# Performance work log

Measured on AMD Instinct MI355X. Metric: run time of the kernel, lower is better.

Reference implementation:

```python
import jax, jax.numpy as jnp
import numpy as np

NEG_SLOPE = 0.2  # PyG GATConv default negative_slope


def gat_conv(x, edge_index, W, att_src, att_dst, bias):
    """PyG-style GATConv (concat heads, add_self_loops=True, eval mode).
    x: [N, F_in], edge_index: [2, E] (row 0 = src j, row 1 = dst i).
    W: [F_in, H*C], att_src/att_dst: [H, C], bias: [H*C].
    """
    N = x.shape[0]
    H, C = att_src.shape
    loops = jnp.arange(N, dtype=edge_index.dtype)
    src = jnp.concatenate([edge_index[0], loops])  # [E+N]
    dst = jnp.concatenate([edge_index[1], loops])
    h = (x @ W).reshape(N, H, C)                              # [N,H,C]
    a_src = jnp.einsum('nhc,hc->nh', h, att_src)              # [N,H]
    a_dst = jnp.einsum('nhc,hc->nh', h, att_dst)
    alpha = jax.nn.leaky_relu(a_src[src] + a_dst[dst], NEG_SLOPE)  # [E+N,H]
    # segment softmax over edges sharing the same destination node
    m = jax.ops.segment_max(alpha, dst, num_segments=N)       # [N,H]
    e = jnp.exp(alpha - jax.lax.stop_gradient(m)[dst])
    denom = jax.ops.segment_sum(e, dst, num_segments=N)       # [N,H]
    a = e / (denom[dst] + 1e-16)                              # [E+N,H]
    msg = h[src] * a[:, :, None]                              # [E+N,H,C]
    out = jax.ops.segment_sum(msg, dst, num_segments=N)       # [N,H,C]
    return out.reshape(N, H * C) + bias


def setup_inputs() -> dict:
    key = jax.random.key(0)
    ks = jax.random.split(key, 10)
    N, F, NC, C1, H1 = 50000, 128, 40, 16, 8
    E = 800000
    x = jax.random.normal(ks[0], (N, F), dtype=jnp.float32)
    edge_index = jax.random.randint(ks[1], (2, E), 0, N, dtype=jnp.int64)
    s1 = 1.0 / np.sqrt(F)
    W1 = jax.random.uniform(ks[2], (F, H1 * C1), jnp.float32, -s1, s1)
    att_src1 = jax.random.uniform(ks[3], (H1, C1), jnp.float32, -1.0, 1.0) * s1
    att_dst1 = jax.random.uniform(ks[4], (H1, C1), jnp.float32, -1.0, 1.0) * s1
    bias1 = jnp.zeros((H1 * C1,), jnp.float32)
    s2 = 1.0 / np.sqrt(H1 * C1)
    W2 = jax.random.uniform(ks[5], (H1 * C1, NC), jnp.float32, -s2, s2)
    att_src2 = jax.random.uniform(ks[6], (1, NC), jnp.float32, -1.0, 1.0) * s2
    att_dst2 = jax.random.uniform(ks[7], (1, NC), jnp.float32, -1.0, 1.0) * s2
    bias2 = jnp.zeros((NC,), jnp.float32)
    return {"x": x, "edge_index": edge_index, "W1": W1, "att_src1": att_src1,
            "att_dst1": att_dst1, "bias1": bias1, "W2": W2, "att_src2": att_src2,
            "att_dst2": att_dst2, "bias2": bias2}


def reference(x, edge_index, W1, att_src1, att_dst1, bias1, W2, att_src2, att_dst2, bias2):
    h = gat_conv(x, edge_index, W1, att_src1, att_dst1, bias1)   # [N, 128]
    # dropout in eval mode = identity
    out = gat_conv(h, edge_index, W2, att_src2, att_dst2, bias2)  # [N, 40]
    return out
```

## Files before the change

### kernel.cpp

```cpp
#include <hip/hip_runtime.h>
#include <hip/hip_bf16.h>
#include <math.h>

#define NEG_SLOPE 0.2f
#define WSZ 384
#define GZ  32

typedef __bf16 bf16x8 __attribute__((ext_vector_type(8)));
typedef float f32x4 __attribute__((ext_vector_type(4)));

__device__ __forceinline__ float lrelu(float x) { return x > 0.f ? x : NEG_SLOPE * x; }

__device__ __forceinline__ unsigned short f2bfu(float f) {
    unsigned int ua = __float_as_uint(f);
    return (unsigned short)((ua + 0x7fffu + ((ua >> 16) & 1u)) >> 16);
}
__device__ __forceinline__ float bfu2f(unsigned short u) {
    return __uint_as_float(((unsigned int)u) << 16);
}
__device__ __forceinline__ float bf_lo(unsigned int u) { return __uint_as_float(u << 16); }
__device__ __forceinline__ float bf_hi(unsigned int u) { return __uint_as_float(u & 0xffff0000u); }

__global__ __launch_bounds__(256) void k_prep(const float* __restrict__ W1,
                                              bf16x8* __restrict__ Wp,
                                              const float* __restrict__ W2,
                                              bf16x8* __restrict__ W2p,
                                              const float* __restrict__ att_s1,
                                              const float* __restrict__ att_d1,
                                              const float* __restrict__ att_s2,
                                              const float* __restrict__ att_d2,
                                              int* __restrict__ cnt, int N) {
    int g = blockIdx.x * 256 + threadIdx.x;
    if (g < 2048) {
        int n = g & 15, quad = (g >> 4) & 3, c = (g >> 6) & 3, ct = g >> 8;
        bf16x8 v;
#pragma unroll
        for (int j = 0; j < 8; ++j)
            v[j] = (__bf16)W1[(c * 32 + quad * 8 + j) * 128 + ct * 16 + n];
        Wp[g] = v;
    } else if (g < 2560) {
        int idx = g - 2048;
        int n = idx & 15, quad = (idx >> 4) & 3, c = (idx >> 6) & 3, t8 = idx >> 8;
        int h = n & 7;
        const float* av = (n < 8) ? att_s1 : att_d1;
        bf16x8 vv;
#pragma unroll
        for (int j = 0; j < 8; ++j) {
            int f = c * 32 + quad * 8 + j;
            float full = 0.f;
            for (int cc = 0; cc < 16; ++cc)
                full += W1[f * 128 + h * 16 + cc] * av[h * 16 + cc];
            __bf16 hi = (__bf16)full;
            vv[j] = t8 ? (__bf16)(full - (float)hi) : hi;
        }
        Wp[g] = vv;
    } else if (g < 3328) {
        int idx = g - 2560;
        int n = idx & 15, quad = (idx >> 4) & 3, c = (idx >> 6) & 3, ct = idx >> 8;
        int colc = ct * 16 + n;
        bf16x8 v;
        if (colc < 40) {
#pragma unroll
            for (int j = 0; j < 8; ++j)
                v[j] = (__bf16)W2[(c * 32 + quad * 8 + j) * 40 + colc];
        } else if (ct == 2 && n >= 8 && n < 12) {
            const float* av = (n & 1) ? att_d2 : att_s2;
#pragma unroll
            for (int j = 0; j < 8; ++j) {
                int f = c * 32 + quad * 8 + j;
                float full = 0.f;
                for (int cc = 0; cc < 40; ++cc) full += W2[f * 40 + cc] * av[cc];
                __bf16 hi = (__bf16)full;
                v[j] = (n >= 10) ? (__bf16)(full - (float)hi) : hi;
            }
        } else {
#pragma unroll
            for (int j = 0; j < 8; ++j) v[j] = (__bf16)0.f;
        }
        W2p[idx] = v;
    }
    if (g < N) cnt[g] = 0;
}

__global__ __launch_bounds__(256) void k_hist(const int* __restrict__ ei, int E, int N,
                                              int* __restrict__ cnt,
                                              unsigned short* __restrict__ rank) {
    int e = blockIdx.x * 256 + threadIdx.x;
    if (e >= E + N) return;
    int d = (e < E) ? ei[E + e] : (e - E);
    rank[e] = (unsigned short)atomicAdd(&cnt[d], 1);
}

__global__ __launch_bounds__(256) void k_scan_part(const int* __restrict__ cnt, int N,
                                                   int* __restrict__ psum) {
    __shared__ int sh[256];
    int t = threadIdx.x;
    int base = blockIdx.x * 1024 + t * 4;
    int tl = 0;
#pragma unroll
    for (int j = 0; j < 4; ++j) tl += (base + j < N) ? cnt[base + j] : 0;
    sh[t] = tl; __syncthreads();
    for (int off = 128; off > 0; off >>= 1) {
        if (t < off) sh[t] += sh[t + off];
        __syncthreads();
    }
    if (t == 0) psum[blockIdx.x] = sh[0];
}

__global__ __launch_bounds__(256) void k_scan_add(const int* __restrict__ cnt, int N,
                                                  const int* __restrict__ psum,
                                                  int* __restrict__ rowptr) {
    __shared__ int sh[256];
    __shared__ int basep;
    int t = threadIdx.x;
    if (t == 0) {
        int s = 0;
        for (int i = 0; i < blockIdx.x; ++i) s += psum[i];
        basep = s;
    }
    int base = blockIdx.x * 1024 + t * 4;
    int c[4]; int tl = 0;
#pragma unroll
    for (int j = 0; j < 4; ++j) { c[j] = (base + j < N) ? cnt[base + j] : 0; tl += c[j]; }
    sh[t] = tl; __syncthreads();
    for (int off = 1; off < 256; off <<= 1) {
        int a = (t >= off) ? sh[t - off] : 0;
        __syncthreads();
        sh[t] += a;
        __syncthreads();
    }
    int run = basep + (sh[t] - tl);
#pragma unroll
    for (int j = 0; j < 4; ++j) {
        if (base + j < N) {
            rowptr[base + j] = run; run += c[j];
            if (base + j == N - 1) rowptr[N] = run;
        }
    }
}

__global__ __launch_bounds__(256) void k_scatter(const int* __restrict__ ei, int E, int N,
                                                 const int* __restrict__ rowptr,
                                                 const unsigned short* __restrict__ rank,
                                                 unsigned short* __restrict__ col) {
    int e = blockIdx.x * 256 + threadIdx.x;
    if (e >= E + N) return;
    int s, d;
    if (e < E) { s = ei[e]; d = ei[E + e]; } else { s = d = e - E; }
    col[rowptr[d] + (int)rank[e]] = (unsigned short)s;
}

__global__ __launch_bounds__(256) void k_gemm1(const float* __restrict__ x,
                                               const bf16x8* __restrict__ Wp,
                                               unsigned short* __restrict__ h1A,
                                               unsigned short* __restrict__ h1B,
                                               float* __restrict__ a_src,
                                               float* __restrict__ a_dst, int N) {
    int t = threadIdx.x;
    int w = t >> 6, lane = t & 63, quad = lane >> 4, n16 = lane & 15;
    int row0 = blockIdx.x * 64 + w * 16;
    int arow = row0 + n16; if (arow >= N) arow = N - 1;
    const float* px = x + (size_t)arow * 128;

    bf16x8 ah[4], al[4];
#pragma unroll
    for (int c = 0; c < 4; ++c) {
        float4 v0 = *(const float4*)&px[c * 32 + quad * 8];
        float4 v1 = *(const float4*)&px[c * 32 + quad * 8 + 4];
        float xf[8] = {v0.x, v0.y, v0.z, v0.w, v1.x, v1.y, v1.z, v1.w};
#pragma unroll
        for (int j = 0; j < 8; ++j) {
            __bf16 hi = (__bf16)xf[j];
            ah[c][j] = hi;
            al[c][j] = (__bf16)(xf[j] - (float)hi);
        }
    }

    f32x4 acc[10];
#pragma unroll
    for (int ct = 0; ct < 10; ++ct) acc[ct] = (f32x4){0.f, 0.f, 0.f, 0.f};

    const uint4* wp4 = (const uint4*)Wp;
#pragma unroll
    for (int ct = 0; ct < 10; ++ct) {
#pragma unroll
        for (int c = 0; c < 4; ++c) {
            union { uint4 u; bf16x8 b; } bu;
            bu.u = wp4[((ct * 4 + c) * 4 + quad) * 16 + n16];
            acc[ct] = __builtin_amdgcn_mfma_f32_16x16x32_bf16(ah[c], bu.b, acc[ct], 0, 0, 0);
            acc[ct] = __builtin_amdgcn_mfma_f32_16x16x32_bf16(al[c], bu.b, acc[ct], 0, 0, 0);
        }
    }

    int nodeb = row0 + quad * 4;
#pragma unroll
    for (int ct = 0; ct < 8; ++ct) {
        unsigned short* hp = (ct < 4) ? h1A : h1B;
        int chl = (ct & 3) * 16 + n16;
#pragma unroll
        for (int reg = 0; reg < 4; ++reg) {
            int node = nodeb + reg;
            if (node < N) hp[(size_t)node * 64 + chl] = f2bfu(acc[ct][reg]);
        }
    }
#pragma unroll
    for (int reg = 0; reg < 4; ++reg) {
        int node = nodeb + reg;
        float av = acc[8][reg] + acc[9][reg];
        if (node < N) {
            if (n16 < 8) a_src[(size_t)node * 8 + n16] = av;
            else         a_dst[(size_t)node * 8 + (n16 - 8)] = av;
        }
    }
}

__global__ __launch_bounds__(256) void k_aggr1(const int* __restrict__ rowptr,
                                               const unsigned short* __restrict__ col,
                                               const float* __restrict__ a_src,
                                               const float* __restrict__ a_dst,
                                               const unsigned int* __restrict__ h1A,
                                               const unsigned int* __restrict__ h1B,
                                               const float* __restrict__ bias1,
                                               unsigned int* __restrict__ out1h,
                                               unsigned int* __restrict__ out1l,
                                               int N, int nag) {
    __shared__ float4 evL[WSZ + GZ];
    __shared__ int    colL[WSZ + GZ];
    __shared__ int    rpL[9];
    __shared__ float4 adL[8];
    int p = (blockIdx.x >= nag) ? 1 : 0;
    int blk = blockIdx.x - p * nag;
    const uint4* hp4 = (const uint4*)(p ? h1B : h1A);
    int t = threadIdx.x;
    int node0 = blk * 8;
    if (t < 9) {
        int nd = node0 + t; if (nd > N) nd = N;
        rpL[t] = rowptr[nd];
    }
    if (t >= 64 && t < 72) {
        int nd = node0 + (t - 64); if (nd >= N) nd = N - 1;
        adL[t - 64] = *(const float4*)&a_dst[(size_t)nd * 8 + p * 4];
    }
    __syncthreads();
    int w0v = rpL[0], end8 = rpL[8];

    int w = t >> 6, lane = t & 63, half = lane >> 5, u = lane & 31;
    int e4 = u >> 3, v = u & 7, hh = v >> 1;
    int idx8 = w * 2 + half;
    int node = node0 + idx8;
    bool nv = (node < N);
    int beg = rpL[idx8], end = rpL[idx8 + 1];

    float den = 0.f;
    float nm[8];
#pragma unroll
    for (int k = 0; k < 8; ++k) nm[k] = 0.f;

    for (int w0 = w0v; w0 < end8; w0 += WSZ) {
        int wend = w0 + WSZ; if (wend > end8) wend = end8;
        int wsz = wend - w0;
        if (w0 != w0v) __syncthreads();
        for (int s = w0 + t; s < wend; s += 256) {
            int su = (int)col[s];
            int lo2 = 0;
            if (rpL[lo2 + 4] <= s) lo2 += 4;
            if (rpL[lo2 + 2] <= s) lo2 += 2;
            if (rpL[lo2 + 1] <= s) lo2 += 1;
            float4 as4 = *(const float4*)&a_src[(size_t)su * 8 + p * 4];
            float4 ad4 = adL[lo2];
            float4 e;
            e.x = __expf(lrelu(as4.x + ad4.x));
            e.y = __expf(lrelu(as4.y + ad4.y));
            e.z = __expf(lrelu(as4.z + ad4.z));
            e.w = __expf(lrelu(as4.w + ad4.w));
            evL[s - w0] = e;
            colL[s - w0] = su;
        }
        if (t < GZ) {
            colL[wsz + t] = 0;
            evL[wsz + t] = make_float4(0.f, 0.f, 0.f, 0.f);
        }
        __syncthreads();
        int lbeg = (beg > w0) ? beg : w0;
        int lend = (end < wend) ? end : wend;
        int ldeg = lend - lbeg;
        int ldO = __shfl_xor(ldeg, 32);
        int ldm = (ldeg > ldO) ? ldeg : ldO;
        int ob0 = lbeg - w0;
        const float* evf = (const float*)evL;
        for (int c = 0; c < ldm; c += 32) {
            int ccm = ldeg - c;
            if (ccm <= 0) continue;
            if (ccm > 32) ccm = 32;
            int ng = (ccm + 3) >> 2;
            int ob = ob0 + c;
            uint4 U0 = hp4[colL[ob + e4] * 8 + v];
            uint4 U1 = hp4[colL[ob + 4 + e4] * 8 + v];
            uint4 U2 = hp4[colL[ob + 8 + e4] * 8 + v];
            uint4 U3 = hp4[colL[ob + 12 + e4] * 8 + v];
            int body = ng - 4;
            int g = 0;
#pragma unroll 2
            for (; g < body; ++g) {
                uint4 UN = hp4[colL[ob + (g + 4) * 4 + e4] * 8 + v];
                int ii = g * 4 + e4;
                float ev = (c + ii < ldeg) ? evf[(ob + ii) * 4 + hh] : 0.f;
                den += ev;
                nm[0] = fmaf(ev, bf_lo(U0.x), nm[0]);
                nm[1] = fmaf(ev, bf_hi(U0.x), nm[1]);
                nm[2] = fmaf(ev, bf_lo(U0.y), nm[2]);
                nm[3] = fmaf(ev, bf_hi(U0.y), nm[3]);
                nm[4] = fmaf(ev, bf_lo(U0.z), nm[4]);
                nm[5] = fmaf(ev, bf_hi(U0.z), nm[5]);
                nm[6] = fmaf(ev, bf_lo(U0.w), nm[6]);
                nm[7] = fmaf(ev, bf_hi(U0.w), nm[7]);
                U0 = U1; U1 = U2; U2 = U3; U3 = UN;
            }
            for (; g < ng; ++g) {
                int ii = g * 4 + e4;
                float ev = (c + ii < ldeg) ? evf[(ob + ii) * 4 + hh] : 0.f;
                den += ev;
                nm[0] = fmaf(ev, bf_lo(U0.x), nm[0]);
                nm[1] = fmaf(ev, bf_hi(U0.x), nm[1]);
                nm[2] = fmaf(ev, bf_lo(U0.y), nm[2]);
                nm[3] = fmaf(ev, bf_hi(U0.y), nm[3]);
                nm[4] = fmaf(ev, bf_lo(U0.z), nm[4]);
                nm[5] = fmaf(ev, bf_hi(U0.z), nm[5]);
                nm[6] = fmaf(ev, bf_lo(U0.w), nm[6]);
                nm[7] = fmaf(ev, bf_hi(U0.w), nm[7]);
                U0 = U1; U1 = U2; U2 = U3;
            }
        }
    }
    den += __shfl_xor(den, 8);
    den += __shfl_xor(den, 16);
#pragma unroll
    for (int k = 0; k < 8; ++k) {
        nm[k] += __shfl_xor(nm[k], 8);
        nm[k] += __shfl_xor(nm[k], 16);
    }
    if (nv && e4 == 0) {
        float inv = 1.f / (den + 1e-16f);
        float4 b0 = *(const float4*)&bias1[p * 64 + v * 8];
        float4 b1 = *(const float4*)&bias1[p * 64 + v * 8 + 4];
        float bb[8] = {b0.x, b0.y, b0.z, b0.w, b1.x, b1.y, b1.z, b1.w};
        unsigned int H[4], L[4];
#pragma unroll
        for (int q = 0; q < 4; ++q) {
            float o0 = fmaf(nm[2 * q],     inv, bb[2 * q]);
            float o1 = fmaf(nm[2 * q + 1], inv, bb[2 * q + 1]);
            unsigned short h0 = f2bfu(o0), h1 = f2bfu(o1);
            float l0 = o0 - bfu2f(h0), l1 = o1 - bfu2f(h1);
            H[q] = (unsigned int)h0 | ((unsigned int)h1 << 16);
            L[q] = (unsigned int)f2bfu(l0) | ((unsigned int)f2bfu(l1) << 16);
        }
        size_t idx = (size_t)node * 64 + p * 32 + v * 4;
        *(uint4*)&out1h[idx] = make_uint4(H[0], H[1], H[2], H[3]);
        *(uint4*)&out1l[idx] = make_uint4(L[0], L[1], L[2], L[3]);
    }
}

__global__ __launch_bounds__(256) void k_gemm2(const unsigned int* __restrict__ out1h,
                                               const unsigned int* __restrict__ out1l,
                                               const bf16x8* __restrict__ W2p,
                                               unsigned short* __restrict__ h2s,
                                               float* __restrict__ a_src2,
                                               float* __restrict__ a_dst2, int N) {
    int t = threadIdx.x;
    int w = t >> 6, lane = t & 63, quad = lane >> 4, n16 = lane & 15;
    int row0 = blockIdx.x * 64 + w * 16;
    int arow = row0 + n16; if (arow >= N) arow = N - 1;

    bf16x8 ah[4], al[4];
#pragma unroll
    for (int c = 0; c < 4; ++c) {
        size_t base = (size_t)arow * 64 + (c * 32 + quad * 8) / 2;
        union { uint4 u; bf16x8 b; } hu, lu;
        hu.u = *(const uint4*)&out1h[base];
        lu.u = *(const uint4*)&out1l[base];
        ah[c] = hu.b;
        al[c] = lu.b;
    }

    f32x4 acc[3];
#pragma unroll
    for (int ct = 0; ct < 3; ++ct) acc[ct] = (f32x4){0.f, 0.f, 0.f, 0.f};

    const uint4* wp4 = (const uint4*)W2p;
#pragma unroll
    for (int ct = 0; ct < 3; ++ct) {
#pragma unroll
        for (int c = 0; c < 4; ++c) {
            union { uint4 u; bf16x8 b; } bu;
            bu.u = wp4[((ct * 4 + c) * 4 + quad) * 16 + n16];
            acc[ct] = __builtin_amdgcn_mfma_f32_16x16x32_bf16(ah[c], bu.b, acc[ct], 0, 0, 0);
            acc[ct] = __builtin_amdgcn_mfma_f32_16x16x32_bf16(al[c], bu.b, acc[ct], 0, 0, 0);
        }
    }

    int nodeb = row0 + quad * 4;
#pragma unroll
    for (int reg = 0; reg < 4; ++reg) {
        int node = nodeb + reg;
#pragma unroll
        for (int ct = 0; ct < 3; ++ct) {
            int ch = ct * 16 + n16;
            if (node < N && ch < 40) h2s[(size_t)node * 64 + ch] = f2bfu(acc[ct][reg]);
        }
        float fv = acc[2][reg];
        float fused = fv + __shfl_xor(fv, 2);
        if (node < N) {
            if (n16 == 8) a_src2[node] = fused;
            else if (n16 == 9) a_dst2[node] = fused;
        }
    }
}

__global__ __launch_bounds__(256) void k_aggr2(const int* __restrict__ rowptr,
                                               const unsigned short* __restrict__ col,
                                               const float* __restrict__ a_src2,
                                               const float* __restrict__ a_dst2,
                                               const unsigned int* __restrict__ h2b,
                                               const float* __restrict__ bias2,
                                               float* __restrict__ out, int N) {
    __shared__ float evL[WSZ + GZ];
    __shared__ int   colL[WSZ + GZ];
    __shared__ int   rpL[9];
    __shared__ float adL[8];
    int t = threadIdx.x;
    int node0 = blockIdx.x * 8;
    if (t < 9) {
        int nd = node0 + t; if (nd > N) nd = N;
        rpL[t] = rowptr[nd];
    }
    if (t >= 64 && t < 72) {
        int nd = node0 + (t - 64); if (nd >= N) nd = N - 1;
        adL[t - 64] = a_dst2[nd];
    }
    __syncthreads();
    int w0v = rpL[0], end8 = rpL[8];

    int w = t >> 6, lane = t & 63, half = lane >> 5, u = lane & 31;
    int e4 = u >> 3, v = u & 7;
    int idx8 = w * 2 + half;
    int node = node0 + idx8;
    bool nv = (node < N);
    int beg = rpL[idx8], end = rpL[idx8 + 1];

    const uint4* h24 = (const uint4*)h2b;
    float den = 0.f;
    float am[8];
#pragma unroll
    for (int k = 0; k < 8; ++k) am[k] = 0.f;

    for (int w0 = w0v; w0 < end8; w0 += WSZ) {
        int wend = w0 + WSZ; if (wend > end8) wend = end8;
        int wsz = wend - w0;
        if (w0 != w0v) __syncthreads();
        for (int s = w0 + t; s < wend; s += 256) {
            int su = (int)col[s];
            int lo2 = 0;
            if (rpL[lo2 + 4] <= s) lo2 += 4;
            if (rpL[lo2 + 2] <= s) lo2 += 2;
            if (rpL[lo2 + 1] <= s) lo2 += 1;
            evL[s - w0] = __expf(lrelu(a_src2[su] + adL[lo2]));
            colL[s - w0] = su;
        }
        if (t < GZ) {
            colL[wsz + t] = 0;
            evL[wsz + t] = 0.f;
        }
        __syncthreads();
        int lbeg = (beg > w0) ? beg : w0;
        int lend = (end < wend) ? end : wend;
        int ldeg = lend - lbeg;
        int ldO = __shfl_xor(ldeg, 32);
        int ldm = (ldeg > ldO) ? ldeg : ldO;
        int ob0 = lbeg - w0;
        for (int c = 0; c < ldm; c += 32) {
            int ccm = ldeg - c;
            if (ccm <= 0) continue;
            if (ccm > 32) ccm = 32;
            int ng = (ccm + 3) >> 2;
            int ob = ob0 + c;
            uint4 U0 = h24[colL[ob + e4] * 8 + v];
            uint4 U1 = h24[colL[ob + 4 + e4] * 8 + v];
            uint4 U2 = h24[colL[ob + 8 + e4] * 8 + v];
            uint4 U3 = h24[colL[ob + 12 + e4] * 8 + v];
            int body = ng - 4;
            int g = 0;
#pragma unroll 2
            for (; g < body; ++g) {
                uint4 UN = h24[colL[ob + (g + 4) * 4 + e4] * 8 + v];
                int ii = g * 4 + e4;
                float evv = (c + ii < ldeg) ? evL[ob + ii] : 0.f;
                den += evv;
                am[0] = fmaf(evv, bf_lo(U0.x), am[0]);
                am[1] = fmaf(evv, bf_hi(U0.x), am[1]);
                am[2] = fmaf(evv, bf_lo(U0.y), am[2]);
                am[3] = fmaf(evv, bf_hi(U0.y), am[3]);
                am[4] = fmaf(evv, bf_lo(U0.z), am[4]);
                am[5] = fmaf(evv, bf_hi(U0.z), am[5]);
                am[6] = fmaf(evv, bf_lo(U0.w), am[6]);
                am[7] = fmaf(evv, bf_hi(U0.w), am[7]);
                U0 = U1; U1 = U2; U2 = U3; U3 = UN;
            }
            for (; g < ng; ++g) {
                int ii = g * 4 + e4;
                float evv = (c + ii < ldeg) ? evL[ob + ii] : 0.f;
                den += evv;
                am[0] = fmaf(evv, bf_lo(U0.x), am[0]);
                am[1] = fmaf(evv, bf_hi(U0.x), am[1]);
                am[2] = fmaf(evv, bf_lo(U0.y), am[2]);
                am[3] = fmaf(evv, bf_hi(U0.y), am[3]);
                am[4] = fmaf(evv, bf_lo(U0.z), am[4]);
                am[5] = fmaf(evv, bf_hi(U0.z), am[5]);
                am[6] = fmaf(evv, bf_lo(U0.w), am[6]);
                am[7] = fmaf(evv, bf_hi(U0.w), am[7]);
                U0 = U1; U1 = U2; U2 = U3;
            }
        }
    }
    den += __shfl_xor(den, 8);
    den += __shfl_xor(den, 16);
#pragma unroll
    for (int k = 0; k < 8; ++k) {
        am[k] += __shfl_xor(am[k], 8);
        am[k] += __shfl_xor(am[k], 16);
    }
    if (nv && e4 == 0 && v < 5) {
        float inv = 1.f / (den + 1e-16f);
        float4 b0 = *(const float4*)&bias2[v * 8];
        float4 b1 = *(const float4*)&bias2[v * 8 + 4];
        float4 o0 = make_float4(fmaf(am[0], inv, b0.x), fmaf(am[1], inv, b0.y),
                                fmaf(am[2], inv, b0.z), fmaf(am[3], inv, b0.w));
        float4 o1 = make_float4(fmaf(am[4], inv, b1.x), fmaf(am[5], inv, b1.y),
                                fmaf(am[6], inv, b1.z), fmaf(am[7], inv, b1.w));
        size_t ob = (size_t)node * 40 + v * 8;
        *(float4*)&out[ob] = o0;
        *(float4*)&out[ob + 4] = o1;
    }
}

extern "C" void kernel_launch(void* const* d_in, const int* in_sizes, int n_in,
                              void* d_out, int out_size, void* d_ws, size_t ws_size,
                              hipStream_t stream) {
    const float* x   = (const float*)d_in[0];
    const int*   ei  = (const int*)d_in[1];
    const float* W1  = (const float*)d_in[2];
    const float* as1 = (const float*)d_in[3];
    const float* ad1 = (const float*)d_in[4];
    const float* b1  = (const float*)d_in[5];
    const float* W2  = (const float*)d_in[6];
    const float* as2 = (const float*)d_in[7];
    const float* ad2 = (const float*)d_in[8];
    const float* b2  = (const float*)d_in[9];

    int N = in_sizes[0] / 128;
    int E = in_sizes[1] / 2;
    int EN = E + N;
    size_t Np = (size_t)((N + 3) & ~3);
    size_t ENp = ((size_t)EN + 3) & ~3;

    float* ws = (float*)d_ws;
    unsigned int* out1h = (unsigned int*)ws; ws += Np * 64;
    unsigned int* out1l = (unsigned int*)ws; ws += Np * 64;
    unsigned int* h1A = (unsigned int*)ws; ws += Np * 32;
    unsigned int* h1Bp = (unsigned int*)ws; ws += Np * 32;
    unsigned int* h2b = (unsigned int*)ws; ws += Np * 32;
    float* a_src1  = ws; ws += Np * 8;
    float* a_dst1  = ws; ws += Np * 8;
    float* a_src2v = ws; ws += Np;
    float* a_dst2v = ws; ws += Np;
    bf16x8* Wp  = (bf16x8*)ws; ws += 2560 * 4;
    bf16x8* W2p = (bf16x8*)ws; ws += 768 * 4;
    int* cnt    = (int*)ws; ws += Np;
    int* rowptr = (int*)ws; ws += Np + 4;
    int* psum   = (int*)ws; ws += 256;
    unsigned short* col  = (unsigned short*)ws; ws += ENp / 2 + 4;
    unsigned short* rank = (unsigned short*)ws; ws += ENp / 2 + 4;

    int nb = (N + 1023) / 1024;
    int npre = (N > 3328 ? N : 3328);

    k_prep<<<(npre + 255) / 256, 256, 0, stream>>>(W1, Wp, W2, W2p,
                                                   as1, ad1, as2, ad2, cnt, N);
    k_gemm1<<<(N + 63) / 64, 256, 0, stream>>>(x, Wp,
                                               (unsigned short*)h1A, (unsigned short*)h1Bp,
                                               a_src1, a_dst1, N);
    k_hist<<<(EN + 255) / 256, 256, 0, stream>>>(ei, E, N, cnt, rank);
    k_scan_part<<<nb, 256, 0, stream>>>(cnt, N, psum);
    k_scan_add<<<nb, 256, 0, stream>>>(cnt, N, psum, rowptr);
    k_scatter<<<(EN + 255) / 256, 256, 0, stream>>>(ei, E, N, rowptr, rank, col);

    int nag = (N + 7) / 8;
    k_aggr1<<<2 * nag, 256, 0, stream>>>(rowptr, col, a_src1, a_dst1,
                                         h1A, h1Bp, b1, out1h, out1l, N, nag);
    k_gemm2<<<(N + 63) / 64, 256, 0, stream>>>(out1h, out1l, W2p,
                                               (unsigned short*)h2b, a_src2v, a_dst2v, N);
    k_aggr2<<<nag, 256, 0, stream>>>(rowptr, col, a_src2v, a_dst2v, h2b, b2, (float*)d_out, N);
}
```

Measured before the change: 234.9 us.

## Split layer-1 features into per-head planes and aggregate one head per block

gemm1 now writes h1 as eight separate per-head planes of 16 bf16 channels, replacing the two half-width planes of four heads each. aggr1 launches one block per (8-node group, head), giving four times more blocks. Each edge gather is now a 32-byte row, and each wave processes 16 edges at a time with a shallower prefetch. The aim is more parallelism and denser per-head gathers, but it repeats the col/a_src/rowptr reads and exp computations eight times instead of twice, and adds extra shuffle reduction steps.

New measurement: 299.5 us. 27.5% more time.

```diff
diff --git a/kernel.cpp b/kernel.cpp
--- a/kernel.cpp
+++ b/kernel.cpp
@@ -152,10 +152,9 @@
 
 __global__ __launch_bounds__(256) void k_gemm1(const float* __restrict__ x,
                                                const bf16x8* __restrict__ Wp,
-                                               unsigned short* __restrict__ h1A,
-                                               unsigned short* __restrict__ h1B,
+                                               unsigned short* __restrict__ h1E,
                                                float* __restrict__ a_src,
-                                               float* __restrict__ a_dst, int N) {
+                                               float* __restrict__ a_dst, int N, int NpU) {
     int t = threadIdx.x;
     int w = t >> 6, lane = t & 63, quad = lane >> 4, n16 = lane & 15;
     int row0 = blockIdx.x * 64 + w * 16;
@@ -195,12 +194,11 @@
     int nodeb = row0 + quad * 4;
 #pragma unroll
     for (int ct = 0; ct < 8; ++ct) {
-        unsigned short* hp = (ct < 4) ? h1A : h1B;
-        int chl = (ct & 3) * 16 + n16;
+        unsigned short* hp = h1E + (size_t)ct * NpU * 16;
 #pragma unroll
         for (int reg = 0; reg < 4; ++reg) {
             int node = nodeb + reg;
-            if (node < N) hp[(size_t)node * 64 + chl] = f2bfu(acc[ct][reg]);
+            if (node < N) hp[node * 16 + n16] = f2bfu(acc[ct][reg]);
         }
     }
 #pragma unroll
@@ -218,19 +216,18 @@
                                                const unsigned short* __restrict__ col,
                                                const float* __restrict__ a_src,
                                                const float* __restrict__ a_dst,
-                                               const unsigned int* __restrict__ h1A,
-                                               const unsigned int* __restrict__ h1B,
+                                               const unsigned int* __restrict__ h1E,
                                                const float* __restrict__ bias1,
                                                unsigned int* __restrict__ out1h,
                                                unsigned int* __restrict__ out1l,
-                                               int N, int nag) {
-    __shared__ float4 evL[WSZ + GZ];
-    __shared__ int    colL[WSZ + GZ];
-    __shared__ int    rpL[9];
-    __shared__ float4 adL[8];
-    int p = (blockIdx.x >= nag) ? 1 : 0;
-    int blk = blockIdx.x - p * nag;
-    const uint4* hp4 = (const uint4*)(p ? h1B : h1A);
+                                               int N, int NpU) {
+    __shared__ float evL[WSZ + GZ];
+    __shared__ int   colL[WSZ + GZ];
+    __shared__ int   rpL[9];
+    __shared__ float adL[8];
+    int p = blockIdx.x & 7;
+    int blk = blockIdx.x >> 3;
+    const uint4* hp4 = (const uint4*)(h1E + (size_t)p * NpU * 8);
     int t = threadIdx.x;
     int node0 = blk * 8;
     if (t < 9) {
@@ -239,13 +236,13 @@
     }
     if (t >= 64 && t < 72) {
         int nd = node0 + (t - 64); if (nd >= N) nd = N - 1;
-        adL[t - 64] = *(const float4*)&a_dst[(size_t)nd * 8 + p * 4];
+        adL[t - 64] = a_dst[(size_t)nd * 8 + p];
     }
     __syncthreads();
     int w0v = rpL[0], end8 = rpL[8];
 
     int w = t >> 6, lane = t & 63, half = lane >> 5, u = lane & 31;
-    int e4 = u >> 3, v = u & 7, hh = v >> 1;
+    int e16 = u >> 1, v = u & 1;
     int idx8 = w * 2 + half;
     int node = node0 + idx8;
     bool nv = (node < N);
@@ -266,45 +263,30 @@
             if (rpL[lo2 + 4] <= s) lo2 += 4;
             if (rpL[lo2 + 2] <= s) lo2 += 2;
             if (rpL[lo2 + 1] <= s) lo2 += 1;
-            float4 as4 = *(const float4*)&a_src[(size_t)su * 8 + p * 4];
-            float4 ad4 = adL[lo2];
-            float4 e;
-            e.x = __expf(lrelu(as4.x + ad4.x));
-            e.y = __expf(lrelu(as4.y + ad4.y));
-            e.z = __expf(lrelu(as4.z + ad4.z));
-            e.w = __expf(lrelu(as4.w + ad4.w));
-            evL[s - w0] = e;
+            evL[s - w0] = __expf(lrelu(a_src[(size_t)su * 8 + p] + adL[lo2]));
             colL[s - w0] = su;
         }
         if (t < GZ) {
             colL[wsz + t] = 0;
-            evL[wsz + t] = make_float4(0.f, 0.f, 0.f, 0.f);
+            evL[wsz + t] = 0.f;
         }
         __syncthreads();
         int lbeg = (beg > w0) ? beg : w0;
         int lend = (end < wend) ? end : wend;
         int ldeg = lend - lbeg;
-        int ldO = __shfl_xor(ldeg, 32);
-        int ldm = (ldeg > ldO) ? ldeg : ldO;
-        int ob0 = lbeg - w0;
-        const float* evf = (const float*)evL;
-        for (int c = 0; c < ldm; c += 32) {
-            int ccm = ldeg - c;
-            if (ccm <= 0) continue;
-            if (ccm > 32) ccm = 32;
-            int ng = (ccm + 3) >> 2;
-            int ob = ob0 + c;
-            uint4 U0 = hp4[colL[ob + e4] * 8 + v];
-            uint4 U1 = hp4[colL[ob + 4 + e4] * 8 + v];
-            uint4 U2 = hp4[colL[ob + 8 + e4] * 8 + v];
-            uint4 U3 = hp4[colL[ob + 12 + e4] * 8 + v];
-            int body = ng - 4;
+        if (ldeg > 0) {
+            int ob = lbeg - w0;
+            int ng = (ldeg + 15) >> 4;
+            int o1 = (ng > 1) ? 16 : 0;
+            uint4 U0 = hp4[colL[ob + e16] * 2 + v];
+            uint4 U1 = hp4[colL[ob + o1 + e16] * 2 + v];
+            int body = ng - 2;
             int g = 0;
 #pragma unroll 2
             for (; g < body; ++g) {
-                uint4 UN = hp4[colL[ob + (g + 4) * 4 + e4] * 8 + v];
-                int ii = g * 4 + e4;
-                float ev = (c + ii < ldeg) ? evf[(ob + ii) * 4 + hh] : 0.f;
+                uint4 UN = hp4[colL[ob + (g + 2) * 16 + e16] * 2 + v];
+                int ii = g * 16 + e16;
+                float ev = (ii < ldeg) ? evL[ob + ii] : 0.f;
                 den += ev;
                 nm[0] = fmaf(ev, bf_lo(U0.x), nm[0]);
                 nm[1] = fmaf(ev, bf_hi(U0.x), nm[1]);
@@ -314,11 +296,11 @@
                 nm[5] = fmaf(ev, bf_hi(U0.z), nm[5]);
                 nm[6] = fmaf(ev, bf_lo(U0.w), nm[6]);
                 nm[7] = fmaf(ev, bf_hi(U0.w), nm[7]);
-                U0 = U1; U1 = U2; U2 = U3; U3 = UN;
+                U0 = U1; U1 = UN;
             }
             for (; g < ng; ++g) {
-                int ii = g * 4 + e4;
-                float ev = (c + ii < ldeg) ? evf[(ob + ii) * 4 + hh] : 0.f;
+                int ii = g * 16 + e16;
+                float ev = (ii < ldeg) ? evL[ob + ii] : 0.f;
                 den += ev;
                 nm[0] = fmaf(ev, bf_lo(U0.x), nm[0]);
                 nm[1] = fmaf(ev, bf_hi(U0.x), nm[1]);
@@ -328,21 +310,27 @@
                 nm[5] = fmaf(ev, bf_hi(U0.z), nm[5]);
                 nm[6] = fmaf(ev, bf_lo(U0.w), nm[6]);
                 nm[7] = fmaf(ev, bf_hi(U0.w), nm[7]);
-                U0 = U1; U1 = U2; U2 = U3;
+                U0 = U1;
             }
         }
     }
+    den += __shfl_xor(den, 2);
+    den += __shfl_xor(den, 4);
     den += __shfl_xor(den, 8);
     den += __shfl_xor(den, 16);
 #pragma unroll
     for (int k = 0; k < 8; ++k) {
-        nm[k] += __shfl_xor(nm[k], 8);
-        nm[k] += __shfl_xor(nm[k], 16);
-    }
-    if (nv && e4 == 0) {
+        float xv = nm[k];
+        xv += __shfl_xor(xv, 2);
+        xv += __shfl_xor(xv, 4);
+        xv += __shfl_xor(xv, 8);
+        xv += __shfl_xor(xv, 16);
+        nm[k] = xv;
+    }
+    if (nv && u < 2) {
         float inv = 1.f / (den + 1e-16f);
-        float4 b0 = *(const float4*)&bias1[p * 64 + v * 8];
-        float4 b1 = *(const float4*)&bias1[p * 64 + v * 8 + 4];
+        float4 b0 = *(const float4*)&bias1[p * 16 + v * 8];
+        float4 b1 = *(const float4*)&bias1[p * 16 + v * 8 + 4];
         float bb[8] = {b0.x, b0.y, b0.z, b0.w, b1.x, b1.y, b1.z, b1.w};
         unsigned int H[4], L[4];
 #pragma unroll
@@ -354,7 +342,7 @@
             H[q] = (unsigned int)h0 | ((unsigned int)h1 << 16);
             L[q] = (unsigned int)f2bfu(l0) | ((unsigned int)f2bfu(l1) << 16);
         }
-        size_t idx = (size_t)node * 64 + p * 32 + v * 4;
+        size_t idx = (size_t)node * 64 + p * 8 + v * 4;
         *(uint4*)&out1h[idx] = make_uint4(H[0], H[1], H[2], H[3]);
         *(uint4*)&out1l[idx] = make_uint4(L[0], L[1], L[2], L[3]);
     }
@@ -565,8 +553,7 @@
     float* ws = (float*)d_ws;
     unsigned int* out1h = (unsigned int*)ws; ws += Np * 64;
     unsigned int* out1l = (unsigned int*)ws; ws += Np * 64;
-    unsigned int* h1A = (unsigned int*)ws; ws += Np * 32;
-    unsigned int* h1Bp = (unsigned int*)ws; ws += Np * 32;
+    unsigned int* h1E = (unsigned int*)ws; ws += Np * 64;
     unsigned int* h2b = (unsigned int*)ws; ws += Np * 32;
     float* a_src1  = ws; ws += Np * 8;
     float* a_dst1  = ws; ws += Np * 8;
@@ -585,17 +572,16 @@
 
     k_prep<<<(npre + 255) / 256, 256, 0, stream>>>(W1, Wp, W2, W2p,
                                                    as1, ad1, as2, ad2, cnt, N);
-    k_gemm1<<<(N + 63) / 64, 256, 0, stream>>>(x, Wp,
-                                               (unsigned short*)h1A, (unsigned short*)h1Bp,
-                                               a_src1, a_dst1, N);
+    k_gemm1<<<(N + 63) / 64, 256, 0, stream>>>(x, Wp, (unsigned short*)h1E,
+                                               a_src1, a_dst1, N, (int)Np);
     k_hist<<<(EN + 255) / 256, 256, 0, stream>>>(ei, E, N, cnt, rank);
     k_scan_part<<<nb, 256, 0, stream>>>(cnt, N, psum);
     k_scan_add<<<nb, 256, 0, stream>>>(cnt, N, psum, rowptr);
     k_scatter<<<(EN + 255) / 256, 256, 0, stream>>>(ei, E, N, rowptr, rank, col);
 
     int nag = (N + 7) / 8;
-    k_aggr1<<<2 * nag, 256, 0, stream>>>(rowptr, col, a_src1, a_dst1,
-                                         h1A, h1Bp, b1, out1h, out1l, N, nag);
+    k_aggr1<<<8 * nag, 256, 0, stream>>>(rowptr, col, a_src1, a_dst1,
+                                         h1E, b1, out1h, out1l, N, (int)Np);
     k_gemm2<<<(N + 63) / 64, 256, 0, stream>>>(out1h, out1l, W2p,
                                                (unsigned short*)h2b, a_src2v, a_dst2v, N);
     k_aggr2<<<nag, 256, 0, stream>>>(rowptr, col, a_src2v, a_dst2v, h2b, b2, (float*)d_out, N);
```
